# Kernel optimization log

Hardware: AMD Instinct MI355X
Metric: run time of the kernel (lower is better)

## Reference

```python
import jax, jax.numpy as jnp
import numpy as np

D_IN = 512
D_OUT = 512


def setup_inputs() -> dict:
    key = jax.random.key(0)
    ks = jax.random.split(key, 7)
    B, S = 4, 4096
    sc = 1.0 / np.sqrt(D_IN)
    return {
        "x": jax.random.normal(ks[0], (B, S, D_IN), dtype=jnp.float32),
        "Wq": jax.random.normal(ks[1], (D_IN, D_OUT), dtype=jnp.float32) * sc,
        "bq": jnp.zeros((D_OUT,), dtype=jnp.float32),
        "Wk": jax.random.normal(ks[2], (D_IN, D_OUT), dtype=jnp.float32) * sc,
        "bk": jnp.zeros((D_OUT,), dtype=jnp.float32),
        "Wv": jax.random.normal(ks[3], (D_IN, D_OUT), dtype=jnp.float32) * sc,
        "bv": jnp.zeros((D_OUT,), dtype=jnp.float32),
    }


def reference(x, Wq, bq, Wk, bk, Wv, bv):
    # Linear projections
    Q = x @ Wq + bq  # [B,S,Do]
    K = x @ Wk + bk
    V = x @ Wv + bv
    # NOTE: original torch code computes `len(K) ** 1 / 2` which is
    # (len(K)**1)/2 = batch_size / 2 due to operator precedence (not sqrt).
    scale = x.shape[0] / 2.0
    scores = jnp.einsum("bsd,btd->bst", Q, K) / scale  # [B,S,S]
    a = jax.nn.softmax(scores, axis=-1)
    Z = jnp.einsum("bst,btd->bsd", a, V)  # [B,S,Do]
    return Z
```

## Files before the change

### kernel.cpp

```cpp
#include <hip/hip_runtime.h>

typedef _Float16 h8 __attribute__((ext_vector_type(8)));
typedef float f4 __attribute__((ext_vector_type(4)));

#define MFMA16(a, b, c) __builtin_amdgcn_mfma_f32_16x16x32_f16((a), (b), (c), 0, 0, 0)

__device__ static inline void gl_lds16(const void* g, void* l) {
  __builtin_amdgcn_global_load_lds((const __attribute__((address_space(1))) unsigned int*)g,
                                   (__attribute__((address_space(3))) unsigned int*)l, 16, 0, 0);
}

__device__ static inline unsigned encf(float f) {
  unsigned u = __float_as_uint(f);
  return (u & 0x80000000u) ? ~u : (u | 0x80000000u);
}
__device__ static inline float decf(unsigned u) {
  return __uint_as_float((u & 0x80000000u) ? (u ^ 0x80000000u) : ~u);
}


__global__ void wconv_kernel(const float* __restrict__ Wq, const float* __restrict__ Wk,
                             const float* __restrict__ Wv, _Float16* __restrict__ Wt,
                             unsigned* __restrict__ mEnc) {
  int idx = blockIdx.x * 256 + threadIdx.x;
  if (idx < 16384) mEnc[idx] = 0u;
  int z = idx >> 15, rem = idx & 32767;
  int n = rem >> 6, k0 = (rem & 63) << 3;
  const float* W = (z == 0) ? Wq : (z == 1) ? Wk : Wv;
  float sc = (z == 0) ? 0.5f : 1.0f;
  h8 v;
#pragma unroll
  for (int j = 0; j < 8; ++j) v[j] = (_Float16)(W[(k0 + j) * 512 + n] * sc);
  size_t blk = (size_t)((z * 4 + (n >> 7)) * 8 + (k0 >> 6));
  int off = (n & 127) * 64 + ((((k0 >> 3) & 7) ^ (n & 7)) << 3);
  *(h8*)&Wt[blk * 8192 + off] = v;
}

__global__ __launch_bounds__(256, 3)
void proj_kernel(const float* __restrict__ x, const _Float16* __restrict__ Wt,
                 const float* __restrict__ bq, const float* __restrict__ bk,
                 const float* __restrict__ bv,
                 char* __restrict__ Qimg, char* __restrict__ Kimg, char* __restrict__ VTimg) {
  __shared__ _Float16 sMem[16384];
  _Float16* sA = sMem;
  _Float16* sB = sMem + 8192;
  const int tid = threadIdx.x;
  const int wave = tid >> 6, lane = tid & 63;
  const int quad = lane >> 4, lr = lane & 15;
  const int mbase = blockIdx.x * 128, nbase = blockIdx.y * 128, z = blockIdx.z;
  const int sr = tid >> 1, sseg = tid & 1;
  const int rbase = (wave & 1) * 64, cbase = (wave >> 1) * 64;
  const char* WtB = (const char*)Wt + ((size_t)(z * 4 + (nbase >> 7)) * 8) * 16384;

  float4 ax[8];
  f4 acc[4][4];
#pragma unroll
  for (int i = 0; i < 4; ++i)
#pragma unroll
    for (int j = 0; j < 4; ++j) { f4 zz = {0.f, 0.f, 0.f, 0.f}; acc[i][j] = zz; }

  {
    const float4* asrc = (const float4*)&x[(size_t)(mbase + sr) * 512 + sseg * 32];
#pragma unroll
    for (int i = 0; i < 8; ++i) ax[i] = asrc[i];
#pragma unroll
    for (int j = 0; j < 4; ++j)
      gl_lds16(WtB + tid * 16 + j * 4096, (char*)sB + tid * 16 + j * 4096);
  }

  for (int kt = 0; kt < 8; ++kt) {
    if (kt > 0) __syncthreads();
#pragma unroll
    for (int i = 0; i < 4; ++i) {
      h8 v;
      float4 f0 = ax[2 * i], f1 = ax[2 * i + 1];
      v[0] = (_Float16)f0.x; v[1] = (_Float16)f0.y; v[2] = (_Float16)f0.z; v[3] = (_Float16)f0.w;
      v[4] = (_Float16)f1.x; v[5] = (_Float16)f1.y; v[6] = (_Float16)f1.z; v[7] = (_Float16)f1.w;
      *(h8*)&sA[sr * 64 + (((sseg * 4 + i) ^ (sr & 7)) << 3)] = v;
    }
    if (kt > 0) {
#pragma unroll
      for (int j = 0; j < 4; ++j)
        gl_lds16(WtB + kt * 16384 + tid * 16 + j * 4096, (char*)sB + tid * 16 + j * 4096);
    }
    __syncthreads();
    if (kt < 7) {
      const float4* asrc = (const float4*)&x[(size_t)(mbase + sr) * 512 + (kt + 1) * 64 + sseg * 32];
#pragma unroll
      for (int i = 0; i < 8; ++i) ax[i] = asrc[i];
    }
#pragma unroll
    for (int ks = 0; ks < 2; ++ks) {
      h8 a[4], bb[4];
#pragma unroll
      for (int rt = 0; rt < 4; ++rt) {
        const int r = rbase + rt * 16 + lr;
        a[rt] = *(const h8*)&sA[r * 64 + ((((ks << 2) | quad) ^ (lr & 7)) << 3)];
      }
#pragma unroll
      for (int ct = 0; ct < 4; ++ct) {
        const int r = cbase + ct * 16 + lr;
        bb[ct] = *(const h8*)&sB[r * 64 + ((((ks << 2) | quad) ^ (lr & 7)) << 3)];
      }
#pragma unroll
      for (int rt = 0; rt < 4; ++rt)
#pragma unroll
        for (int ct = 0; ct < 4; ++ct)
          acc[rt][ct] = MFMA16(a[rt], bb[ct], acc[rt][ct]);
    }
  }

  const float* bias = (z == 0) ? bq : (z == 1) ? bk : bv;
  const float bscale = (z == 0) ? 0.5f : 1.0f;
  _Float16* sC = sMem;
  __syncthreads();
#pragma unroll
  for (int ct = 0; ct < 4; ++ct) {
    const int dl = cbase + ct * 16 + lr;
    const float bb = bias[nbase + dl] * bscale;
#pragma unroll
    for (int rt = 0; rt < 4; ++rt) {
#pragma unroll
      for (int r = 0; r < 4; ++r) {
        const int sl = rbase + rt * 16 + quad * 4 + r;
        const _Float16 val = (_Float16)(acc[rt][ct][r] + bb);
        if (z == 2) {
          sC[((sl >> 6) << 13) + dl * 64 + ((((sl >> 3) & 7) ^ (dl & 7)) << 3) + (sl & 7)] = val;
        } else {
          sC[((dl >> 6) << 13) + sl * 64 + ((((dl >> 3) & 7) ^ (sl & 7)) << 3) + (dl & 7)] = val;
        }
      }
    }
  }
  __syncthreads();
  const int b_ = mbase >> 12;
  char* dst;
  if (z != 2) {
    char* img = (z == 0) ? Qimg : Kimg;
    dst = img + ((size_t)((b_ * 32 + ((mbase & 4095) >> 7)) * 8 + (nbase >> 6) + (tid >> 7))) * 16384;
  } else {
    dst = VTimg + ((size_t)((b_ * 4 + (nbase >> 7)) * 64 + ((mbase & 4095) >> 6) + (tid >> 7))) * 16384;
  }
  dst += (size_t)(tid & 127) * 128;
#pragma unroll
  for (int k = 0; k < 8; ++k)
    *(int4*)(dst + k * 16) = *(const int4*)&sC[tid * 64 + k * 8];
}

__global__ __launch_bounds__(256, 3)
void qk_kernel(const char* __restrict__ Qimg, const char* __restrict__ Kimg,
               char* __restrict__ S, unsigned* __restrict__ mEnc, int b0, int s0) {
  __shared__ _Float16 sMem[16384];
  _Float16* sA = sMem;
  _Float16* sB = sMem + 8192;
  const int tid = threadIdx.x;
  const int wave = tid >> 6, lane = tid & 63;
  const int quad = lane >> 4, lr = lane & 15;
  const int cb = blockIdx.x;
  const int rbL = blockIdx.z * gridDim.y + blockIdx.y;
  const int b = b0 + blockIdx.z;
  const int rbase = (wave & 1) * 64, cbase = (wave >> 1) * 64;
  const char* Ab = Qimg + ((size_t)((b * 32 + (s0 >> 7) + blockIdx.y) * 8)) * 16384;
  const char* Bb = Kimg + ((size_t)((b * 32 + cb) * 8)) * 16384;

  f4 acc[4][4];
#pragma unroll
  for (int i = 0; i < 4; ++i)
#pragma unroll
    for (int j = 0; j < 4; ++j) { f4 zz = {0.f, 0.f, 0.f, 0.f}; acc[i][j] = zz; }

#pragma unroll
  for (int j = 0; j < 4; ++j) {
    gl_lds16(Ab + tid * 16 + j * 4096, (char*)sA + tid * 16 + j * 4096);
    gl_lds16(Bb + tid * 16 + j * 4096, (char*)sB + tid * 16 + j * 4096);
  }

  for (int kt = 0; kt < 8; ++kt) {
    asm volatile("s_waitcnt vmcnt(0)" ::: "memory");
    __builtin_amdgcn_s_barrier();
    __builtin_amdgcn_sched_barrier(0);
    h8 a[4][2], bb[4][2];
#pragma unroll
    for (int ks = 0; ks < 2; ++ks) {
#pragma unroll
      for (int rt = 0; rt < 4; ++rt) {
        const int r = rbase + rt * 16 + lr;
        a[rt][ks] = *(const h8*)&sA[r * 64 + ((((ks << 2) | quad) ^ (lr & 7)) << 3)];
      }
#pragma unroll
      for (int ct = 0; ct < 4; ++ct) {
        const int r = cbase + ct * 16 + lr;
        bb[ct][ks] = *(const h8*)&sB[r * 64 + ((((ks << 2) | quad) ^ (lr & 7)) << 3)];
      }
    }
    asm volatile("s_waitcnt lgkmcnt(0)" ::: "memory");
    __builtin_amdgcn_s_barrier();
    __builtin_amdgcn_sched_barrier(0);
    if (kt < 7) {
#pragma unroll
      for (int j = 0; j < 4; ++j) {
        gl_lds16(Ab + (kt + 1) * 16384 + tid * 16 + j * 4096, (char*)sA + tid * 16 + j * 4096);
        gl_lds16(Bb + (kt + 1) * 16384 + tid * 16 + j * 4096, (char*)sB + tid * 16 + j * 4096);
      }
    }
    __builtin_amdgcn_s_setprio(1);
#pragma unroll
    for (int ks = 0; ks < 2; ++ks)
#pragma unroll
      for (int rt = 0; rt < 4; ++rt)
#pragma unroll
        for (int ct = 0; ct < 4; ++ct)
          acc[rt][ct] = MFMA16(a[rt][ks], bb[ct][ks], acc[rt][ct]);
    __builtin_amdgcn_s_setprio(0);
  }

  {
    const int growb = b * 4096 + s0 + blockIdx.y * 128;
#pragma unroll
    for (int rt = 0; rt < 4; ++rt) {
#pragma unroll
      for (int r = 0; r < 4; ++r) {
        float mx = fmaxf(fmaxf(acc[rt][0][r], acc[rt][1][r]),
                         fmaxf(acc[rt][2][r], acc[rt][3][r]));
        mx = fmaxf(mx, __shfl_xor(mx, 1));
        mx = fmaxf(mx, __shfl_xor(mx, 2));
        mx = fmaxf(mx, __shfl_xor(mx, 4));
        mx = fmaxf(mx, __shfl_xor(mx, 8));
        if (lr == 0)
          atomicMax(&mEnc[growb + rbase + rt * 16 + quad * 4 + r], encf(mx));
      }
    }
  }

  _Float16* sC = sMem;
  __syncthreads();
#pragma unroll
  for (int ct = 0; ct < 4; ++ct) {
    const int tl = cbase + ct * 16 + lr;
#pragma unroll
    for (int rt = 0; rt < 4; ++rt) {
#pragma unroll
      for (int r = 0; r < 4; ++r) {
        const int sl = rbase + rt * 16 + quad * 4 + r;
        sC[((tl >> 6) << 13) + sl * 64 + ((((tl >> 3) & 7) ^ (sl & 7)) << 3) + (tl & 7)] =
            (_Float16)acc[rt][ct][r];
      }
    }
  }
  __syncthreads();
  char* dst = S + ((size_t)(rbL * 64 + cb * 2 + (tid >> 7))) * 16384 + (size_t)(tid & 127) * 128;
#pragma unroll
  for (int k = 0; k < 8; ++k)
    *(int4*)(dst + k * 16) = *(const int4*)&sC[tid * 64 + k * 8];
}

__global__ __launch_bounds__(512, 2)
void pv_kernel(const char* __restrict__ S, const char* __restrict__ VTimg,
               const unsigned* __restrict__ mEnc, float* __restrict__ out,
               int b0, int s0, int nyb, int nb) {
  __shared__ _Float16 sMem[73728];
  __shared__ float ls[64];
  const int tid = threadIdx.x;
  const int wave = tid >> 6, lane = tid & 63;
  const int quad = lane >> 4, lr = lane & 15;
  const int flat = blockIdx.x;
  int bL, yl;
  if (nb == 4) { bL = (flat & 7) >> 1; yl = ((flat >> 3) << 1) | (flat & 1); }
  else { bL = flat / nyb; yl = flat - bL * nyb; }
  const int b = b0 + bL;
  const int sbL = bL * nyb + yl;
  const int rbase = (wave & 1) * 32, cbase = (wave >> 1) * 128;
  const char* Ab = S + ((size_t)((sbL >> 1) * 64)) * 16384 + (size_t)(sbL & 1) * 8192;
  const char* Bb = VTimg + ((size_t)(b * 4) * 64) * 16384;

  const int lrow = tid >> 3;
  const int growb = b * 4096 + s0 + yl * 64;
  const float m0 = decf(mEnc[growb + lrow]);
  float rs = 0.f;

  f4 acc[2][8];
#pragma unroll
  for (int i = 0; i < 2; ++i)
#pragma unroll
    for (int j = 0; j < 8; ++j) { f4 zz = {0.f, 0.f, 0.f, 0.f}; acc[i][j] = zz; }

  {
    h8 ha = *(const h8*)(Ab + tid * 16);
#pragma unroll
    for (int j = 0; j < 8; ++j)
      gl_lds16(Bb + (size_t)(j >> 1) * 1048576 + (j & 1) * 8192 + tid * 16,
               (char*)sMem + 16384 + j * 8192 + tid * 16);
    h8 w;
#pragma unroll
    for (int u = 0; u < 8; ++u) { float e = __expf((float)ha[u] - m0); w[u] = (_Float16)e; rs += e; }
    *(h8*)((char*)sMem + tid * 16) = w;
    asm volatile("s_waitcnt vmcnt(0) lgkmcnt(0)" ::: "memory");
    __builtin_amdgcn_s_barrier();
    __builtin_amdgcn_sched_barrier(0);
  }

  for (int kt = 0; kt < 64; ++kt) {
    const int cur = kt & 1;
    _Float16* sA = sMem + cur * 4096;
    _Float16* sB = sMem + 8192 + cur * 32768;
    char* sAn = (char*)sMem + (cur ^ 1) * 8192;
    char* sBn = (char*)sMem + 16384 + (cur ^ 1) * 65536;
    const bool more = (kt < 63);
    h8 han;
    if (more) {
      han = *(const h8*)(Ab + (kt + 1) * 16384 + tid * 16);
#pragma unroll
      for (int j = 0; j < 8; ++j)
        gl_lds16(Bb + (size_t)(j >> 1) * 1048576 + (size_t)(kt + 1) * 16384 + (j & 1) * 8192 + tid * 16,
                 sBn + j * 8192 + tid * 16);
    }
    {
      h8 a[2], bbf[8];
#pragma unroll
      for (int rt = 0; rt < 2; ++rt) {
        const int r = rbase + rt * 16 + lr;
        a[rt] = *(const h8*)&sA[r * 64 + (((quad) ^ (lr & 7)) << 3)];
      }
#pragma unroll
      for (int ct = 0; ct < 8; ++ct) {
        const int d = cbase + ct * 16 + lr;
        bbf[ct] = *(const h8*)&sB[d * 64 + (((quad) ^ (lr & 7)) << 3)];
      }
      __builtin_amdgcn_s_setprio(1);
#pragma unroll
      for (int rt = 0; rt < 2; ++rt)
#pragma unroll
        for (int ct = 0; ct < 8; ++ct)
          acc[rt][ct] = MFMA16(a[rt], bbf[ct], acc[rt][ct]);
      __builtin_amdgcn_s_setprio(0);
    }
    if (more) {
      h8 w;
#pragma unroll
      for (int u = 0; u < 8; ++u) { float e = __expf((float)han[u] - m0); w[u] = (_Float16)e; rs += e; }
      *(h8*)(sAn + tid * 16) = w;
    }
    {
      h8 a[2], bbf[8];
#pragma unroll
      for (int rt = 0; rt < 2; ++rt) {
        const int r = rbase + rt * 16 + lr;
        a[rt] = *(const h8*)&sA[r * 64 + (((4 | quad) ^ (lr & 7)) << 3)];
      }
#pragma unroll
      for (int ct = 0; ct < 8; ++ct) {
        const int d = cbase + ct * 16 + lr;
        bbf[ct] = *(const h8*)&sB[d * 64 + (((4 | quad) ^ (lr & 7)) << 3)];
      }
      __builtin_amdgcn_s_setprio(1);
#pragma unroll
      for (int rt = 0; rt < 2; ++rt)
#pragma unroll
        for (int ct = 0; ct < 8; ++ct)
          acc[rt][ct] = MFMA16(a[rt], bbf[ct], acc[rt][ct]);
      __builtin_amdgcn_s_setprio(0);
    }
    asm volatile("s_waitcnt vmcnt(0) lgkmcnt(0)" ::: "memory");
    __builtin_amdgcn_s_barrier();
    __builtin_amdgcn_sched_barrier(0);
  }

  rs += __shfl_xor(rs, 1); rs += __shfl_xor(rs, 2); rs += __shfl_xor(rs, 4);
  if ((tid & 7) == 0) ls[lrow] = rs;
  __syncthreads();

#pragma unroll
  for (int rt = 0; rt < 2; ++rt) {
#pragma unroll
    for (int r = 0; r < 4; ++r) {
      const int lrw = rbase + rt * 16 + quad * 4 + r;
      const int srow = s0 + yl * 64 + lrw;
      const float li = 1.0f / ls[lrw];
      float* op = &out[((size_t)b * 4096 + srow) * 512];
#pragma unroll
      for (int ct = 0; ct < 8; ++ct)
        op[cbase + ct * 16 + lr] = acc[rt][ct][r] * li;
    }
  }
}

extern "C" void kernel_launch(void* const* d_in, const int* in_sizes, int n_in,
                              void* d_out, int out_size, void* d_ws, size_t ws_size,
                              hipStream_t stream) {
  (void)in_sizes; (void)n_in; (void)out_size;
  const float* x  = (const float*)d_in[0];
  const float* Wq = (const float*)d_in[1];
  const float* bq = (const float*)d_in[2];
  const float* Wk = (const float*)d_in[3];
  const float* bk = (const float*)d_in[4];
  const float* Wv = (const float*)d_in[5];
  const float* bv = (const float*)d_in[6];
  float* out = (float*)d_out;
  char* ws = (char*)d_ws;
  char* Qimg  = ws;
  char* Kimg  = ws + ((size_t)16 << 20);
  char* VTimg = ws + ((size_t)32 << 20);
  _Float16* Wt = (_Float16*)(ws + ((size_t)48 << 20));
  unsigned* mEnc = (unsigned*)(ws + ((size_t)50 << 20) - 65536);
  char* Simg   = ws + ((size_t)50 << 20);

  wconv_kernel<<<dim3(384), dim3(256), 0, stream>>>(Wq, Wk, Wv, Wt, mEnc);
  proj_kernel<<<dim3(128, 4, 3), dim3(256), 0, stream>>>(x, Wt, bq, bk, bv, Qimg, Kimg, VTimg);

  const size_t avail = ws_size > ((size_t)50 << 20) ? ws_size - ((size_t)50 << 20) : 0;
  int nchunk, nb, Ms;
  if      (avail >= ((size_t)128 << 20)) { nchunk = 1;  nb = 4; Ms = 4096; }
  else if (avail >= ((size_t)64  << 20)) { nchunk = 2;  nb = 2; Ms = 4096; }
  else if (avail >= ((size_t)32  << 20)) { nchunk = 4;  nb = 1; Ms = 4096; }
  else if (avail >= ((size_t)16  << 20)) { nchunk = 8;  nb = 1; Ms = 2048; }
  else if (avail >= ((size_t)8   << 20)) { nchunk = 16; nb = 1; Ms = 1024; }
  else                                   { nchunk = 32; nb = 1; Ms = 512;  }
  const int chunksPerBatch = 4096 / Ms;
  const int nyb = Ms / 64;

  for (int c = 0; c < nchunk; ++c) {
    int b0, s0;
    if (nb > 1 || Ms == 4096) { b0 = c * nb; s0 = 0; }
    else { b0 = c / chunksPerBatch; s0 = (c % chunksPerBatch) * Ms; }
    qk_kernel<<<dim3(32, Ms / 128, nb), dim3(256), 0, stream>>>(Qimg, Kimg, Simg, mEnc, b0, s0);
    pv_kernel<<<dim3(nb * nyb), dim3(512), 0, stream>>>(Simg, VTimg, mEnc, out, b0, s0, nyb, nb);
  }
}
```

Before: 377.0 us.

## Prefetch score tiles two steps ahead and reduce row-max atomics via LDS

In the PV kernel, the raw score tile loads now run two iterations ahead using nontemporal loads, with a partial vmcnt wait so the A-tile global latency overlaps more compute. The score kernel merges per-wave row maxima through shared memory before issuing one atomicMax per row, which halves the global atomics. Output stores become nontemporal. The cost is extra barriers in the score kernel, more registers for the prefetched tile, and fragile hand-counted waitcnt values.

```diff
diff --git a/kernel.cpp b/kernel.cpp
--- a/kernel.cpp
+++ b/kernel.cpp
@@ -214,26 +214,37 @@
     __builtin_amdgcn_s_setprio(0);
   }
 
-  {
-    const int growb = b * 4096 + s0 + blockIdx.y * 128;
-#pragma unroll
-    for (int rt = 0; rt < 4; ++rt) {
-#pragma unroll
-      for (int r = 0; r < 4; ++r) {
-        float mx = fmaxf(fmaxf(acc[rt][0][r], acc[rt][1][r]),
-                         fmaxf(acc[rt][2][r], acc[rt][3][r]));
-        mx = fmaxf(mx, __shfl_xor(mx, 1));
-        mx = fmaxf(mx, __shfl_xor(mx, 2));
-        mx = fmaxf(mx, __shfl_xor(mx, 4));
-        mx = fmaxf(mx, __shfl_xor(mx, 8));
-        if (lr == 0)
-          atomicMax(&mEnc[growb + rbase + rt * 16 + quad * 4 + r], encf(mx));
-      }
-    }
-  }
+  float mxv[4][4];
+#pragma unroll
+  for (int rt = 0; rt < 4; ++rt) {
+#pragma unroll
+    for (int r = 0; r < 4; ++r) {
+      float mx = fmaxf(fmaxf(acc[rt][0][r], acc[rt][1][r]),
+                       fmaxf(acc[rt][2][r], acc[rt][3][r]));
+      mx = fmaxf(mx, __shfl_xor(mx, 1));
+      mx = fmaxf(mx, __shfl_xor(mx, 2));
+      mx = fmaxf(mx, __shfl_xor(mx, 4));
+      mx = fmaxf(mx, __shfl_xor(mx, 8));
+      mxv[rt][r] = mx;
+    }
+  }
+  __syncthreads();
+  float* rmf = (float*)sMem;
+  if (lr == 0) {
+#pragma unroll
+    for (int rt = 0; rt < 4; ++rt)
+#pragma unroll
+      for (int r = 0; r < 4; ++r)
+        rmf[(wave >> 1) * 128 + rbase + rt * 16 + quad * 4 + r] = mxv[rt][r];
+  }
+  __syncthreads();
+  if (tid < 128) {
+    const float v = fmaxf(rmf[tid], rmf[128 + tid]);
+    atomicMax(&mEnc[b * 4096 + s0 + blockIdx.y * 128 + tid], encf(v));
+  }
+  __syncthreads();
 
   _Float16* sC = sMem;
-  __syncthreads();
 #pragma unroll
   for (int ct = 0; ct < 4; ++ct) {
     const int tl = cbase + ct * 16 + lr;
@@ -274,8 +285,7 @@
   const char* Bb = VTimg + ((size_t)(b * 4) * 64) * 16384;
 
   const int lrow = tid >> 3;
-  const int growb = b * 4096 + s0 + yl * 64;
-  const float m0 = decf(mEnc[growb + lrow]);
+  const float m0 = decf(mEnc[b * 4096 + s0 + yl * 64 + lrow]);
   float rs = 0.f;
 
   f4 acc[2][8];
@@ -284,17 +294,20 @@
 #pragma unroll
     for (int j = 0; j < 8; ++j) { f4 zz = {0.f, 0.f, 0.f, 0.f}; acc[i][j] = zz; }
 
+  h8 han;
   {
-    h8 ha = *(const h8*)(Ab + tid * 16);
+    h8 ha = __builtin_nontemporal_load((const h8*)(Ab + tid * 16));
 #pragma unroll
     for (int j = 0; j < 8; ++j)
       gl_lds16(Bb + (size_t)(j >> 1) * 1048576 + (j & 1) * 8192 + tid * 16,
                (char*)sMem + 16384 + j * 8192 + tid * 16);
+    __builtin_amdgcn_sched_barrier(0);
     h8 w;
 #pragma unroll
     for (int u = 0; u < 8; ++u) { float e = __expf((float)ha[u] - m0); w[u] = (_Float16)e; rs += e; }
     *(h8*)((char*)sMem + tid * 16) = w;
-    asm volatile("s_waitcnt vmcnt(0) lgkmcnt(0)" ::: "memory");
+    han = __builtin_nontemporal_load((const h8*)(Ab + 16384 + tid * 16));
+    asm volatile("s_waitcnt vmcnt(1) lgkmcnt(0)" ::: "memory");
     __builtin_amdgcn_s_barrier();
     __builtin_amdgcn_sched_barrier(0);
   }
@@ -303,17 +316,17 @@
     const int cur = kt & 1;
     _Float16* sA = sMem + cur * 4096;
     _Float16* sB = sMem + 8192 + cur * 32768;
-    char* sAn = (char*)sMem + (cur ^ 1) * 8192;
-    char* sBn = (char*)sMem + 16384 + (cur ^ 1) * 65536;
-    const bool more = (kt < 63);
-    h8 han;
-    if (more) {
-      han = *(const h8*)(Ab + (kt + 1) * 16384 + tid * 16);
+    const bool moreB = (kt < 63), moreA = (kt < 62);
+    if (moreB) {
 #pragma unroll
       for (int j = 0; j < 8; ++j)
         gl_lds16(Bb + (size_t)(j >> 1) * 1048576 + (size_t)(kt + 1) * 16384 + (j & 1) * 8192 + tid * 16,
-                 sBn + j * 8192 + tid * 16);
-    }
+                 (char*)sMem + 16384 + (cur ^ 1) * 65536 + j * 8192 + tid * 16);
+    }
+    __builtin_amdgcn_sched_barrier(0);
+    h8 hanN;
+    if (moreA)
+      hanN = __builtin_nontemporal_load((const h8*)(Ab + (size_t)(kt + 2) * 16384 + tid * 16));
     {
       h8 a[2], bbf[8];
 #pragma unroll
@@ -334,11 +347,11 @@
           acc[rt][ct] = MFMA16(a[rt], bbf[ct], acc[rt][ct]);
       __builtin_amdgcn_s_setprio(0);
     }
-    if (more) {
+    if (moreB) {
       h8 w;
 #pragma unroll
       for (int u = 0; u < 8; ++u) { float e = __expf((float)han[u] - m0); w[u] = (_Float16)e; rs += e; }
-      *(h8*)(sAn + tid * 16) = w;
+      *(h8*)((char*)sMem + (cur ^ 1) * 8192 + tid * 16) = w;
     }
     {
       h8 a[2], bbf[8];
@@ -360,9 +373,14 @@
           acc[rt][ct] = MFMA16(a[rt], bbf[ct], acc[rt][ct]);
       __builtin_amdgcn_s_setprio(0);
     }
-    asm volatile("s_waitcnt vmcnt(0) lgkmcnt(0)" ::: "memory");
+    if (moreA) {
+      asm volatile("s_waitcnt vmcnt(1) lgkmcnt(0)" ::: "memory");
+    } else {
+      asm volatile("s_waitcnt vmcnt(0) lgkmcnt(0)" ::: "memory");
+    }
     __builtin_amdgcn_s_barrier();
     __builtin_amdgcn_sched_barrier(0);
+    if (moreA) han = hanN;
   }
 
   rs += __shfl_xor(rs, 1); rs += __shfl_xor(rs, 2); rs += __shfl_xor(rs, 4);
@@ -379,7 +397,7 @@
       float* op = &out[((size_t)b * 4096 + srow) * 512];
 #pragma unroll
       for (int ct = 0; ct < 8; ++ct)
-        op[cbase + ct * 16 + lr] = acc[rt][ct][r] * li;
+        __builtin_nontemporal_store(acc[rt][ct][r] * li, &op[cbase + ct * 16 + lr]);
     }
   }
 }
```

Measured after the change: 391.6 us. +3.9%, slower.

## Pre-convert x to swizzled fp16 image and pipeline projection with direct LDS loads

Applied to the files above, without the earlier changes.

Adds a kernel that converts x to fp16 in the swizzled tile layout once, so the projection GEMM can stream both operands with global_load_lds instead of loading fp32 into registers and converting three times (once per Q/K/V). The projection loop is restructured to read fragments into registers, barrier, then prefetch the next tile while issuing MFMAs at raised priority, and the grid is reordered so that column blocks sharing an x tile run adjacently. The QK row-max reduction now combines the two column waves through LDS before one atomic per row instead of two. The cost is an extra kernel launch, a 16MB fp16 copy of x, and a larger workspace offset that can push the S-buffer chunking to a smaller configuration when the workspace is limited.

```diff
diff --git a/kernel.cpp b/kernel.cpp
--- a/kernel.cpp
+++ b/kernel.cpp
@@ -36,8 +36,22 @@
   *(h8*)&Wt[blk * 8192 + off] = v;
 }
 
+__global__ void xconv_kernel(const float* __restrict__ x, _Float16* __restrict__ Ximg) {
+  int idx = blockIdx.x * 256 + threadIdx.x;
+  int row = idx >> 6;
+  int k0 = (idx & 63) << 3;
+  const float* src = &x[(size_t)row * 512 + k0];
+  float4 f0 = *(const float4*)src, f1 = *(const float4*)(src + 4);
+  h8 v;
+  v[0] = (_Float16)f0.x; v[1] = (_Float16)f0.y; v[2] = (_Float16)f0.z; v[3] = (_Float16)f0.w;
+  v[4] = (_Float16)f1.x; v[5] = (_Float16)f1.y; v[6] = (_Float16)f1.z; v[7] = (_Float16)f1.w;
+  size_t blk = (size_t)((row >> 7) * 8 + (k0 >> 6));
+  int off = (row & 127) * 64 + ((((k0 >> 3) & 7) ^ (row & 7)) << 3);
+  *(h8*)&Ximg[blk * 8192 + off] = v;
+}
+
 __global__ __launch_bounds__(256, 3)
-void proj_kernel(const float* __restrict__ x, const _Float16* __restrict__ Wt,
+void proj_kernel(const _Float16* __restrict__ Ximg, const _Float16* __restrict__ Wt,
                  const float* __restrict__ bq, const float* __restrict__ bk,
                  const float* __restrict__ bv,
                  char* __restrict__ Qimg, char* __restrict__ Kimg, char* __restrict__ VTimg) {
@@ -47,67 +61,63 @@
   const int tid = threadIdx.x;
   const int wave = tid >> 6, lane = tid & 63;
   const int quad = lane >> 4, lr = lane & 15;
-  const int mbase = blockIdx.x * 128, nbase = blockIdx.y * 128, z = blockIdx.z;
-  const int sr = tid >> 1, sseg = tid & 1;
+  const int nb4 = blockIdx.x;
+  const int mb = blockIdx.y;
+  const int z = blockIdx.z;
+  const int mbase = mb * 128, nbase = nb4 * 128;
   const int rbase = (wave & 1) * 64, cbase = (wave >> 1) * 64;
-  const char* WtB = (const char*)Wt + ((size_t)(z * 4 + (nbase >> 7)) * 8) * 16384;
-
-  float4 ax[8];
+  const char* Ab = (const char*)Ximg + ((size_t)(mb * 8)) * 16384;
+  const char* Bb = (const char*)Wt + ((size_t)((z * 4 + nb4) * 8)) * 16384;
+
   f4 acc[4][4];
 #pragma unroll
   for (int i = 0; i < 4; ++i)
 #pragma unroll
     for (int j = 0; j < 4; ++j) { f4 zz = {0.f, 0.f, 0.f, 0.f}; acc[i][j] = zz; }
 
-  {
-    const float4* asrc = (const float4*)&x[(size_t)(mbase + sr) * 512 + sseg * 32];
-#pragma unroll
-    for (int i = 0; i < 8; ++i) ax[i] = asrc[i];
-#pragma unroll
-    for (int j = 0; j < 4; ++j)
-      gl_lds16(WtB + tid * 16 + j * 4096, (char*)sB + tid * 16 + j * 4096);
+#pragma unroll
+  for (int j = 0; j < 4; ++j) {
+    gl_lds16(Ab + tid * 16 + j * 4096, (char*)sA + tid * 16 + j * 4096);
+    gl_lds16(Bb + tid * 16 + j * 4096, (char*)sB + tid * 16 + j * 4096);
   }
 
   for (int kt = 0; kt < 8; ++kt) {
-    if (kt > 0) __syncthreads();
-#pragma unroll
-    for (int i = 0; i < 4; ++i) {
-      h8 v;
-      float4 f0 = ax[2 * i], f1 = ax[2 * i + 1];
-      v[0] = (_Float16)f0.x; v[1] = (_Float16)f0.y; v[2] = (_Float16)f0.z; v[3] = (_Float16)f0.w;
-      v[4] = (_Float16)f1.x; v[5] = (_Float16)f1.y; v[6] = (_Float16)f1.z; v[7] = (_Float16)f1.w;
-      *(h8*)&sA[sr * 64 + (((sseg * 4 + i) ^ (sr & 7)) << 3)] = v;
-    }
-    if (kt > 0) {
-#pragma unroll
-      for (int j = 0; j < 4; ++j)
-        gl_lds16(WtB + kt * 16384 + tid * 16 + j * 4096, (char*)sB + tid * 16 + j * 4096);
-    }
-    __syncthreads();
-    if (kt < 7) {
-      const float4* asrc = (const float4*)&x[(size_t)(mbase + sr) * 512 + (kt + 1) * 64 + sseg * 32];
-#pragma unroll
-      for (int i = 0; i < 8; ++i) ax[i] = asrc[i];
-    }
+    asm volatile("s_waitcnt vmcnt(0)" ::: "memory");
+    __builtin_amdgcn_s_barrier();
+    __builtin_amdgcn_sched_barrier(0);
+    h8 a[4][2], bb[4][2];
 #pragma unroll
     for (int ks = 0; ks < 2; ++ks) {
-      h8 a[4], bb[4];
 #pragma unroll
       for (int rt = 0; rt < 4; ++rt) {
         const int r = rbase + rt * 16 + lr;
-        a[rt] = *(const h8*)&sA[r * 64 + ((((ks << 2) | quad) ^ (lr & 7)) << 3)];
+        a[rt][ks] = *(const h8*)&sA[r * 64 + ((((ks << 2) | quad) ^ (lr & 7)) << 3)];
       }
 #pragma unroll
       for (int ct = 0; ct < 4; ++ct) {
         const int r = cbase + ct * 16 + lr;
-        bb[ct] = *(const h8*)&sB[r * 64 + ((((ks << 2) | quad) ^ (lr & 7)) << 3)];
-      }
+        bb[ct][ks] = *(const h8*)&sB[r * 64 + ((((ks << 2) | quad) ^ (lr & 7)) << 3)];
+      }
+    }
+    asm volatile("s_waitcnt lgkmcnt(0)" ::: "memory");
+    __builtin_amdgcn_s_barrier();
+    __builtin_amdgcn_sched_barrier(0);
+    if (kt < 7) {
+#pragma unroll
+      for (int j = 0; j < 4; ++j) {
+        gl_lds16(Ab + (kt + 1) * 16384 + tid * 16 + j * 4096, (char*)sA + tid * 16 + j * 4096);
+        gl_lds16(Bb + (kt + 1) * 16384 + tid * 16 + j * 4096, (char*)sB + tid * 16 + j * 4096);
+      }
+    }
+    __builtin_amdgcn_s_setprio(1);
+#pragma unroll
+    for (int ks = 0; ks < 2; ++ks)
 #pragma unroll
       for (int rt = 0; rt < 4; ++rt)
 #pragma unroll
         for (int ct = 0; ct < 4; ++ct)
-          acc[rt][ct] = MFMA16(a[rt], bb[ct], acc[rt][ct]);
-    }
+          acc[rt][ct] = MFMA16(a[rt][ks], bb[ct][ks], acc[rt][ct]);
+    __builtin_amdgcn_s_setprio(0);
   }
 
   const float* bias = (z == 0) ? bq : (z == 1) ? bk : bv;
@@ -214,26 +224,37 @@
     __builtin_amdgcn_s_setprio(0);
   }
 
-  {
-    const int growb = b * 4096 + s0 + blockIdx.y * 128;
-#pragma unroll
-    for (int rt = 0; rt < 4; ++rt) {
-#pragma unroll
-      for (int r = 0; r < 4; ++r) {
-        float mx = fmaxf(fmaxf(acc[rt][0][r], acc[rt][1][r]),
-                         fmaxf(acc[rt][2][r], acc[rt][3][r]));
-        mx = fmaxf(mx, __shfl_xor(mx, 1));
-        mx = fmaxf(mx, __shfl_xor(mx, 2));
-        mx = fmaxf(mx, __shfl_xor(mx, 4));
-        mx = fmaxf(mx, __shfl_xor(mx, 8));
-        if (lr == 0)
-          atomicMax(&mEnc[growb + rbase + rt * 16 + quad * 4 + r], encf(mx));
-      }
-    }
-  }
+  float mxv[4][4];
+#pragma unroll
+  for (int rt = 0; rt < 4; ++rt) {
+#pragma unroll
+    for (int r = 0; r < 4; ++r) {
+      float mx = fmaxf(fmaxf(acc[rt][0][r], acc[rt][1][r]),
+                       fmaxf(acc[rt][2][r], acc[rt][3][r]));
+      mx = fmaxf(mx, __shfl_xor(mx, 1));
+      mx = fmaxf(mx, __shfl_xor(mx, 2));
+      mx = fmaxf(mx, __shfl_xor(mx, 4));
+      mx = fmaxf(mx, __shfl_xor(mx, 8));
+      mxv[rt][r] = mx;
+    }
+  }
+  __syncthreads();
+  float* rmf = (float*)sMem;
+  if (lr == 0) {
+#pragma unroll
+    for (int rt = 0; rt < 4; ++rt)
+#pragma unroll
+      for (int r = 0; r < 4; ++r)
+        rmf[(wave >> 1) * 128 + rbase + rt * 16 + quad * 4 + r] = mxv[rt][r];
+  }
+  __syncthreads();
+  if (tid < 128) {
+    const float v = fmaxf(rmf[tid], rmf[128 + tid]);
+    atomicMax(&mEnc[b * 4096 + s0 + blockIdx.y * 128 + tid], encf(v));
+  }
+  __syncthreads();
 
   _Float16* sC = sMem;
-  __syncthreads();
 #pragma unroll
   for (int ct = 0; ct < 4; ++ct) {
     const int tl = cbase + ct * 16 + lr;
@@ -274,8 +295,7 @@
   const char* Bb = VTimg + ((size_t)(b * 4) * 64) * 16384;
 
   const int lrow = tid >> 3;
-  const int growb = b * 4096 + s0 + yl * 64;
-  const float m0 = decf(mEnc[growb + lrow]);
+  const float m0 = decf(mEnc[b * 4096 + s0 + yl * 64 + lrow]);
   float rs = 0.f;
 
   f4 acc[2][8];
@@ -402,12 +422,14 @@
   char* VTimg = ws + ((size_t)32 << 20);
   _Float16* Wt = (_Float16*)(ws + ((size_t)48 << 20));
   unsigned* mEnc = (unsigned*)(ws + ((size_t)50 << 20) - 65536);
-  char* Simg   = ws + ((size_t)50 << 20);
+  _Float16* Ximg = (_Float16*)(ws + ((size_t)50 << 20));
+  char* Simg   = ws + ((size_t)66 << 20);
 
   wconv_kernel<<<dim3(384), dim3(256), 0, stream>>>(Wq, Wk, Wv, Wt, mEnc);
-  proj_kernel<<<dim3(128, 4, 3), dim3(256), 0, stream>>>(x, Wt, bq, bk, bv, Qimg, Kimg, VTimg);
-
-  const size_t avail = ws_size > ((size_t)50 << 20) ? ws_size - ((size_t)50 << 20) : 0;
+  xconv_kernel<<<dim3(4096), dim3(256), 0, stream>>>(x, Ximg);
+  proj_kernel<<<dim3(4, 128, 3), dim3(256), 0, stream>>>(Ximg, Wt, bq, bk, bv, Qimg, Kimg, VTimg);
+
+  const size_t avail = ws_size > ((size_t)66 << 20) ? ws_size - ((size_t)66 << 20) : 0;
   int nchunk, nb, Ms;
   if      (avail >= ((size_t)128 << 20)) { nchunk = 1;  nb = 4; Ms = 4096; }
   else if (avail >= ((size_t)64  << 20)) { nchunk = 2;  nb = 2; Ms = 4096; }
```

Measured after the change: 378.4 us. Within noise of the previous version (+0.4%).
